# Optimization experiments

Measured on AMD Instinct MI355X. Metric: run time of the kernel, lower is better.

Reference implementation:

```python
import jax, jax.numpy as jnp
import numpy as np
from jax import lax

G, K, KS = 4, 16, 3            # stripes, latents per stripe, support kernel
TEMP, TOPK_RATIO, GATE, EPS = 0.125, 0.125, 0.05, 1e-6


def _l2norm(v):
    # F.normalize(p=2, dim=-1): divide by max(norm, 1e-12)
    return v / jnp.maximum(jnp.linalg.norm(v, axis=-1, keepdims=True), 1e-12)


def _avg_pool3(x):
    # 3x3 avg pool, stride 1, pad 1, count_include_pad=True (torch default)
    s = lax.reduce_window(x, 0.0, lax.add, (1, 1, KS, KS), (1, 1, 1, 1),
                          [(0, 0), (0, 0), (KS // 2, KS // 2), (KS // 2, KS // 2)])
    return s / float(KS * KS)


def setup_inputs() -> dict:
    key = jax.random.key(0)
    k1, k2 = jax.random.split(key)
    x = jax.random.normal(k1, (64, 256, 64, 44), dtype=jnp.float32)
    latent_basis = jax.random.normal(k2, (G, K, 256), dtype=jnp.float32) * 0.05
    return {"x": x, "latent_basis": latent_basis}


def reference(x, latent_basis):
    n, c, h, w = x.shape
    hs = h // G
    # 'n c (g hs) w -> (n g) c hs w'
    sf = x.reshape(n, c, G, hs, w).transpose(0, 2, 1, 3, 4).reshape(n * G, c, hs, w)
    support_feat = _avg_pool3(sf)
    feat_flat = sf.reshape(n, G, c, hs * w).transpose(0, 1, 3, 2)          # n g p c
    supp_flat = support_feat.reshape(n, G, c, hs * w).transpose(0, 1, 3, 2)  # n g p c
    # active mask from detached energy
    e = jnp.mean(lax.stop_gradient(sf) ** 2, axis=1)                       # [n*G, hs, w]
    e = e / jnp.maximum(jnp.max(e, axis=(-2, -1), keepdims=True), EPS)
    am = (e > GATE).astype(jnp.float32)
    fb = (e > 0).astype(jnp.float32)
    use_fb = jnp.sum(am, axis=(-2, -1), keepdims=True) <= 0
    am = jnp.where(use_fb, fb, am).reshape(n, G, hs * w)                   # n g p
    # routing
    sfn = _l2norm(supp_flat)
    lb = _l2norm(latent_basis)                                             # g k c
    logits = jnp.einsum('ngpc,gkc->ngpk', sfn, lb) / TEMP
    route = jax.nn.softmax(logits, axis=-1)
    supp = route * am[..., None]                                           # n g p k
    pw = supp / jnp.maximum(jnp.sum(supp, axis=2, keepdims=True), EPS)
    tokens = jnp.einsum('ngpk,ngpc->ngkc', pw, feat_flat)                  # n g k c
    tokens = tokens.transpose(0, 3, 1, 2).reshape(n, c, G * K)             # n c (g k)
    # presence via top-k over positions
    p = supp.shape[2]
    topk = max(1, min(p, int(p * TOPK_RATIO)))
    vals = lax.top_k(supp.transpose(0, 1, 3, 2), topk)[0]                  # n g k topk
    pres = jnp.mean(vals, axis=-1).reshape(n, G * K)
    pres = pres / jnp.maximum(jnp.sum(pres, axis=1, keepdims=True), EPS)
    return tokens, pres
```

## Files before the change

### kernel.cpp

```cpp
#include <hip/hip_runtime.h>
#include <cstdint>


#define C_ 256
#define W_ 44
#define P_ 704
#define CH_STRIDE 2816
#define NB_STRIDE 720896
#define TOPK_ 88
#define GATE_ 0.05f
#define EPS_ 1e-6f

#define DPP_WAVE_SHL1 0x130
#define DPP_WAVE_SHR1 0x138
__device__ __forceinline__ float dpp_from_left(float v) {
  return __int_as_float(__builtin_amdgcn_update_dpp(
      0, __float_as_int(v), DPP_WAVE_SHR1, 0xF, 0xF, true));
}
__device__ __forceinline__ float dpp_from_right(float v) {
  return __int_as_float(__builtin_amdgcn_update_dpp(
      0, __float_as_int(v), DPP_WAVE_SHL1, 0xF, 0xF, true));
}

__global__ __launch_bounds__(256) void k_norm_basis(const float* __restrict__ lb,
                                                    float* __restrict__ lbn) {
  int gk = blockIdx.x;
  int t = threadIdx.x;
  float v = lb[gk * 256 + t];
  float ss = v * v;
  #pragma unroll
  for (int off = 32; off >= 1; off >>= 1) ss += __shfl_xor(ss, off);
  __shared__ float red[4];
  if ((t & 63) == 0) red[t >> 6] = ss;
  __syncthreads();
  float tot = red[0] + red[1] + red[2] + red[3];
  float scale = 1.f / fmaxf(sqrtf(tot), 1e-12f);
  int g = gk >> 4, k = gk & 15;
  lbn[((g * 256 + t) << 4) + k] = v * scale;
}

__global__ __launch_bounds__(256) void k_route_dot(const float* __restrict__ x,
                                                   const float* __restrict__ lbn,
                                                   float* __restrict__ pd0,
                                                   float* __restrict__ pd1,
                                                   float* __restrict__ sqpw) {
  const int tid = threadIdx.x;
  const int wq = tid >> 6;
  const int l = tid & 63;
  const bool act = (l < 44);
  const int bid = blockIdx.x;
  const int s = bid >> 3;
  const int rem = bid & 7;
  const int q = rem >> 1, half = rem & 1;
  const int w = q * 4 + wq;
  const int n = s >> 2, g = s & 3;
  const int p = w * 44 + l;

  const int lsafe = act ? l : 0;
  const float* xb = x + (size_t)n * NB_STRIDE + (size_t)(half * 128) * CH_STRIDE
                      + (g * 16 + w) * 44 + lsafe;
  const float* xm = xb + ((w > 0)  ? -44 : 0);
  const float* xp = xb + ((w < 15) ?  44 : 0);
  const bool hm = (w > 0), hp = (w < 15);

  const float* lbb = lbn + (g << 12) + (half << 11);

  float rawdot[16];
  #pragma unroll
  for (int k = 0; k < 16; k++) rawdot[k] = 0.f;
  float sq = 0.f, pw2 = 0.f;

  for (int c = 0; c < 128; c += 4) {
    float vm[4], v0[4], vp[4];
    #pragma unroll
    for (int j = 0; j < 4; j++) {
      const size_t o = (size_t)(c + j) * CH_STRIDE;
      vm[j] = xm[o]; v0[j] = xb[o]; vp[j] = xp[o];
    }
    #pragma unroll
    for (int j = 0; j < 4; j++) {
      float a  = act ? v0[j] : 0.f;
      float am_ = (act && hm) ? vm[j] : 0.f;
      float ap_ = (act && hp) ? vp[j] : 0.f;
      float vs = am_ + a + ap_;
      float lf = dpp_from_left(vs);
      float rt = dpp_from_right(vs);
      float win = lf + vs + rt;
      pw2 = fmaf(win, win, pw2);
      sq  = fmaf(a, a, sq);
      const int co = __builtin_amdgcn_readfirstlane((c + j) << 4);
      const float4* wp4 = (const float4*)(lbb + co);
      float4 w0 = wp4[0], w1 = wp4[1], w2 = wp4[2], w3 = wp4[3];
      rawdot[0]  = fmaf(a, w0.x, rawdot[0]);  rawdot[1]  = fmaf(a, w0.y, rawdot[1]);
      rawdot[2]  = fmaf(a, w0.z, rawdot[2]);  rawdot[3]  = fmaf(a, w0.w, rawdot[3]);
      rawdot[4]  = fmaf(a, w1.x, rawdot[4]);  rawdot[5]  = fmaf(a, w1.y, rawdot[5]);
      rawdot[6]  = fmaf(a, w1.z, rawdot[6]);  rawdot[7]  = fmaf(a, w1.w, rawdot[7]);
      rawdot[8]  = fmaf(a, w2.x, rawdot[8]);  rawdot[9]  = fmaf(a, w2.y, rawdot[9]);
      rawdot[10] = fmaf(a, w2.z, rawdot[10]); rawdot[11] = fmaf(a, w2.w, rawdot[11]);
      rawdot[12] = fmaf(a, w3.x, rawdot[12]); rawdot[13] = fmaf(a, w3.y, rawdot[13]);
      rawdot[14] = fmaf(a, w3.z, rawdot[14]); rawdot[15] = fmaf(a, w3.w, rawdot[15]);
    }
  }

  if (act) {
    float* dst = (half ? pd1 : pd0) + (size_t)s * 11264 + p * 16;
    #pragma unroll
    for (int kq = 0; kq < 4; kq++)
      ((float4*)dst)[kq] = make_float4(rawdot[kq*4+0], rawdot[kq*4+1],
                                       rawdot[kq*4+2], rawdot[kq*4+3]);
    *(float2*)(sqpw + ((size_t)(s * 2 + half) * 704 + p) * 2) = make_float2(sq, pw2);
  }
}

__global__ __launch_bounds__(1024) void k_route_fin(float* __restrict__ supp_kp,
                                                    float* __restrict__ supp_pk,
                                                    const float* __restrict__ sqpw,
                                                    float* __restrict__ invden_ws) {
  __shared__ float rsl[11264];
  __shared__ float redA[16];
  __shared__ float redB[16];
  __shared__ float redM[2];
  __shared__ float red2[16 * 16];

  const int tid = threadIdx.x;
  const int w = tid >> 6;
  const int l = tid & 63;
  const bool act = (l < 44);
  const int s = blockIdx.x;
  const int p = w * 44 + l;

  float sq = 0.f, pw2 = 0.f;
  if (act) {
    const float4* a0 = (const float4*)(supp_kp + (size_t)s * 11264 + p * 16);
    const float4* a1 = (const float4*)(supp_pk + (size_t)s * 11264 + p * 16);
    #pragma unroll
    for (int kq = 0; kq < 4; kq++) {
      float4 u = a0[kq], v = a1[kq];
      rsl[(kq*4+0) * 704 + p] = u.x + v.x;
      rsl[(kq*4+1) * 704 + p] = u.y + v.y;
      rsl[(kq*4+2) * 704 + p] = u.z + v.z;
      rsl[(kq*4+3) * 704 + p] = u.w + v.w;
    }
    float2 s0 = *(const float2*)(sqpw + ((size_t)(s * 2 + 0) * 704 + p) * 2);
    float2 s1 = *(const float2*)(sqpw + ((size_t)(s * 2 + 1) * 704 + p) * 2);
    sq = s0.x + s1.x; pw2 = s0.y + s1.y;
  }
  __syncthreads();

  float pd[16];
  #pragma unroll
  for (int k = 0; k < 16; k++) pd[k] = 0.f;
  if (act) {
    #pragma unroll
    for (int dy = -1; dy <= 1; dy++) {
      int yy = w + dy;
      if (yy < 0 || yy > 15) continue;
      #pragma unroll
      for (int dx = -1; dx <= 1; dx++) {
        int xx = l + dx;
        if (xx < 0 || xx > 43) continue;
        int pp = yy * 44 + xx;
        #pragma unroll
        for (int k = 0; k < 16; k++) pd[k] += rsl[k * 704 + pp];
      }
    }
  }

  float e_raw = sq * (1.f / 256.f);
  float m = e_raw;
  #pragma unroll
  for (int off = 32; off >= 1; off >>= 1) m = fmaxf(m, __shfl_xor(m, off));
  if (l == 0) redA[w] = m;
  __syncthreads();
  if (tid == 0) {
    float mm = redA[0];
    for (int w2 = 1; w2 < 16; w2++) mm = fmaxf(mm, redA[w2]);
    redM[0] = mm;
  }
  __syncthreads();
  float M = fmaxf(redM[0], EPS_);
  float e = e_raw / M;
  float am = (e > GATE_) ? 1.f : 0.f;
  float fb = (e_raw > 0.f) ? 1.f : 0.f;
  float a = am;
  #pragma unroll
  for (int off = 32; off >= 1; off >>= 1) a += __shfl_xor(a, off);
  if (l == 0) redB[w] = a;
  __syncthreads();
  if (tid == 0) {
    float sm = 0.f;
    for (int w2 = 0; w2 < 16; w2++) sm += redB[w2];
    redM[1] = sm;
  }
  __syncthreads();
  if (redM[1] <= 0.f) am = fb;

  float pnorm = sqrtf(pw2) * (1.f / 9.f);
  float invn = 1.f / fmaxf(pnorm, 1e-12f);
  float scl = invn * (8.f / 9.f);
  float li[16];
  float mx = -1e30f;
  #pragma unroll
  for (int k = 0; k < 16; k++) { li[k] = pd[k] * scl; mx = fmaxf(mx, li[k]); }
  float ssum = 0.f;
  #pragma unroll
  for (int k = 0; k < 16; k++) { li[k] = __expf(li[k] - mx); ssum += li[k]; }
  float rs2 = am / ssum;
  float supp[16];
  #pragma unroll
  for (int k = 0; k < 16; k++) supp[k] = li[k] * rs2;

  if (act) {
    float* sbp = supp_kp + (size_t)s * (16 * 704);
    #pragma unroll
    for (int k = 0; k < 16; k++) sbp[k * 704 + p] = supp[k];
    float* spk = supp_pk + ((size_t)s * 704 + p) * 16;
    #pragma unroll
    for (int kq = 0; kq < 4; kq++)
      ((float4*)spk)[kq] = make_float4(supp[kq*4+0], supp[kq*4+1],
                                       supp[kq*4+2], supp[kq*4+3]);
  }

  #pragma unroll
  for (int k = 0; k < 16; k++) {
    float v2 = act ? supp[k] : 0.f;
    #pragma unroll
    for (int off = 32; off >= 1; off >>= 1) v2 += __shfl_xor(v2, off);
    if (l == 0) red2[w * 16 + k] = v2;
  }
  __syncthreads();
  if (tid < 16) {
    float den = 0.f;
    for (int w2 = 0; w2 < 16; w2++) den += red2[w2 * 16 + tid];
    invden_ws[s * 16 + tid] = 1.f / fmaxf(den, EPS_);
  }
}

__global__ __launch_bounds__(256) void k_topk(const float* __restrict__ supp_kp,
                                              float* __restrict__ presraw) {
  const int blk = blockIdx.x;
  const int t = threadIdx.x;
  const int lane = t & 63, w = t >> 6;
  const float* v = supp_kp + (size_t)blk * 704;
  const bool h2 = (t < 192);
  uint32_t key0 = __float_as_uint(v[t]);
  uint32_t key1 = __float_as_uint(v[t + 256]);
  uint32_t key2 = h2 ? __float_as_uint(v[t + 512]) : 0u;

  __shared__ uint32_t hist[256];
  __shared__ uint32_t sarr[257];
  __shared__ uint32_t wsum[4];
  __shared__ uint32_t bc0, bc1;
  uint32_t prefix = 0, remaining = TOPK_;

  for (int b = 3; b >= 0; b--) {
    hist[t] = 0u;
    __syncthreads();
    const int shift = b * 8;
    uint32_t mhi = (b == 3) ? 0u : (0xFFFFFFFFu << (shift + 8));
    if ((key0 & mhi) == (prefix & mhi)) atomicAdd(&hist[(key0 >> shift) & 255u], 1u);
    if ((key1 & mhi) == (prefix & mhi)) atomicAdd(&hist[(key1 >> shift) & 255u], 1u);
    if (h2 && ((key2 & mhi) == (prefix & mhi))) atomicAdd(&hist[(key2 >> shift) & 255u], 1u);
    __syncthreads();

    uint32_t val = hist[t];
    #pragma unroll
    for (int off = 1; off < 64; off <<= 1) {
      uint32_t o = (uint32_t)__shfl_down((int)val, off);
      if (lane + off < 64) val += o;
    }
    if (lane == 0) wsum[w] = val;
    __syncthreads();
    uint32_t add = 0;
    for (int w2 = w + 1; w2 < 4; w2++) add += wsum[w2];
    sarr[t] = val + add;
    if (t == 0) sarr[256] = 0u;
    __syncthreads();
    uint32_t s_t = sarr[t], s_n = sarr[t + 1];
    if (s_t >= remaining && s_n < remaining) {
      bc0 = prefix | ((uint32_t)t << shift);
      bc1 = remaining - s_n;
    }
    __syncthreads();
    prefix = bc0; remaining = bc1;
    __syncthreads();
  }

  float tf = __uint_as_float(prefix);
  float sgt = 0.f;
  uint32_t cgt = 0;
  if (key0 > prefix) { sgt += __uint_as_float(key0); cgt++; }
  if (key1 > prefix) { sgt += __uint_as_float(key1); cgt++; }
  if (h2 && key2 > prefix) { sgt += __uint_as_float(key2); cgt++; }
  #pragma unroll
  for (int off = 32; off >= 1; off >>= 1) {
    sgt += __shfl_xor(sgt, off);
    cgt += __shfl_xor(cgt, off);
  }
  __shared__ float rsx[4];
  __shared__ uint32_t rcx[4];
  if (lane == 0) { rsx[w] = sgt; rcx[w] = cgt; }
  __syncthreads();
  if (t == 0) {
    float stot = rsx[0] + rsx[1] + rsx[2] + rsx[3];
    uint32_t ctot = rcx[0] + rcx[1] + rcx[2] + rcx[3];
    float top = stot + (float)(TOPK_ - ctot) * tf;
    presraw[blk] = top * (1.f / (float)TOPK_);
  }
}

__global__ __launch_bounds__(512, 4) void k_tokens(const float* __restrict__ x,
                                                   const float* __restrict__ supp_pk,
                                                   const float* __restrict__ invden,
                                                   float* __restrict__ out) {
  __shared__ float xl[4096];
  const int tid = threadIdx.x;
  const int bid = blockIdx.x;
  const int s = bid >> 1, chalf = bid & 1;
  const int n = s >> 2, g = s & 3;
  const int cl = tid & 127;
  const int q = tid >> 7;
  const int sblk = s * (704 * 16);

  const float* xs = x + (size_t)n * NB_STRIDE + (size_t)(chalf * 128) * CH_STRIDE + g * P_;

  const int li0 = tid, li1 = tid + 512;
  const int lc0 = li0 >> 3, lj0 = li0 & 7;
  const int lc1 = li1 >> 3, lj1 = li1 & 7;
  const float* gp0 = xs + (size_t)lc0 * CH_STRIDE + lj0 * 4;
  const float* gp1 = xs + (size_t)lc1 * CH_STRIDE + lj1 * 4;
  const int wo0 = lc0 * 32 + ((lj0 * 4) ^ ((lc0 & 7) * 4));
  const int wo1 = lc1 * 32 + ((lj1 * 4) ^ ((lc1 & 7) * 4));

  const int sw = (cl & 7) * 4;
  const int rbase = cl * 32;

  float acc[16];
  #pragma unroll
  for (int k = 0; k < 16; k++) acc[k] = 0.f;

  float4 r0 = *(const float4*)gp0;
  float4 r1 = *(const float4*)gp1;
  *(float4*)&xl[wo0] = r0;
  *(float4*)&xl[wo1] = r1;
  __syncthreads();

  for (int tt = 0; tt < 22; tt++) {
    const int p0 = tt * 32;
    float4 n0, n1;
    if (tt < 21) {
      n0 = *(const float4*)(gp0 + p0 + 32);
      n1 = *(const float4*)(gp1 + p0 + 32);
    }

    #pragma unroll
    for (int jj = 0; jj < 8; jj += 4) {
      const int pp0 = q * 8 + jj;
      float4 xv = *(const float4*)&xl[rbase + (pp0 ^ sw)];
      float xa[4] = {xv.x, xv.y, xv.z, xv.w};
      #pragma unroll
      for (int dj = 0; dj < 4; dj++) {
        int uofs = __builtin_amdgcn_readfirstlane(sblk + (p0 + pp0 + dj) * 16);
        const float4* sp = (const float4*)(supp_pk + uofs);
        float4 s0 = sp[0], s1 = sp[1], s2 = sp[2], s3 = sp[3];
        float a = xa[dj];
        acc[0]  += a * s0.x; acc[1]  += a * s0.y; acc[2]  += a * s0.z; acc[3]  += a * s0.w;
        acc[4]  += a * s1.x; acc[5]  += a * s1.y; acc[6]  += a * s1.z; acc[7]  += a * s1.w;
        acc[8]  += a * s2.x; acc[9]  += a * s2.y; acc[10] += a * s2.z; acc[11] += a * s2.w;
        acc[12] += a * s3.x; acc[13] += a * s3.y; acc[14] += a * s3.z; acc[15] += a * s3.w;
      }
    }

    __syncthreads();
    if (tt < 21) {
      *(float4*)&xl[wo0] = n0;
      *(float4*)&xl[wo1] = n1;
      __syncthreads();
    }
  }

  if (q >= 2) {
    float* dst = &xl[((q - 2) * 128 + cl) * 16];
    #pragma unroll
    for (int kq = 0; kq < 4; kq++)
      ((float4*)dst)[kq] = make_float4(acc[kq*4], acc[kq*4+1], acc[kq*4+2], acc[kq*4+3]);
  }
  __syncthreads();
  if (q < 2) {
    const float* src = &xl[(q * 128 + cl) * 16];
    #pragma unroll
    for (int k = 0; k < 16; k++) acc[k] += src[k];
  }
  __syncthreads();
  if (q == 1) {
    float* dst = &xl[cl * 16];
    #pragma unroll
    for (int kq = 0; kq < 4; kq++)
      ((float4*)dst)[kq] = make_float4(acc[kq*4], acc[kq*4+1], acc[kq*4+2], acc[kq*4+3]);
  }
  __syncthreads();
  if (q == 0) {
    const float* src = &xl[cl * 16];
    float* op = out + ((size_t)(n * 256 + chalf * 128 + cl) * 64) + g * 16;
    #pragma unroll
    for (int kq = 0; kq < 4; kq++) {
      int u = __builtin_amdgcn_readfirstlane(s * 16 + kq * 4);
      const float4 iv = *(const float4*)(invden + u);
      float4 o;
      o.x = (acc[kq*4+0] + src[kq*4+0]) * iv.x;
      o.y = (acc[kq*4+1] + src[kq*4+1]) * iv.y;
      o.z = (acc[kq*4+2] + src[kq*4+2]) * iv.z;
      o.w = (acc[kq*4+3] + src[kq*4+3]) * iv.w;
      ((float4*)op)[kq] = o;
    }
  }
}

__global__ __launch_bounds__(64) void k_pres(const float* __restrict__ presraw,
                                             float* __restrict__ out) {
  const int n = blockIdx.x, t = threadIdx.x;
  float v = presraw[n * 64 + t];
  float ssum = v;
  #pragma unroll
  for (int off = 32; off >= 1; off >>= 1) ssum += __shfl_xor(ssum, off);
  out[1048576 + n * 64 + t] = v / fmaxf(ssum, EPS_);
}

extern "C" void kernel_launch(void* const* d_in, const int* in_sizes, int n_in,
                              void* d_out, int out_size, void* d_ws, size_t ws_size,
                              hipStream_t stream) {
  (void)in_sizes; (void)n_in; (void)out_size; (void)ws_size;
  const float* x  = (const float*)d_in[0];
  const float* lb = (const float*)d_in[1];
  float* out = (float*)d_out;
  float* ws = (float*)d_ws;
  float* lbn_ws     = ws;
  float* invden_ws  = ws + 16384;
  float* presraw_ws = ws + 20480;
  float* supp_kp_ws = ws + 24576;
  float* supp_pk_ws = ws + 2908160;
  float* sqpw_ws    = out;

  k_norm_basis<<<64, 256, 0, stream>>>(lb, lbn_ws);
  k_route_dot<<<2048, 256, 0, stream>>>(x, lbn_ws, supp_kp_ws, supp_pk_ws, sqpw_ws);
  k_route_fin<<<256, 1024, 0, stream>>>(supp_kp_ws, supp_pk_ws, sqpw_ws, invden_ws);
  k_topk<<<4096, 256, 0, stream>>>(supp_kp_ws, presraw_ws);
  k_tokens<<<512, 512, 0, stream>>>(x, supp_pk_ws, invden_ws, out);
  k_pres<<<64, 64, 0, stream>>>(presraw_ws, out);
}
```

Baseline: 370.6 us.

## Fuse top-k presence into route_fin and software-pipeline route_dot channel loads

Removes the separate k_topk kernel. Each wave of k_route_fin now runs an 8-bit radix select over one latent's 704 support values. It keeps the values in shared memory and uses a wave-private histogram with shuffle-based scans instead of block-wide barriers. This also drops the global write of the k-major support buffer and its later re-read. Separately, k_route_dot double-buffers its channel-group loads and adds an occupancy hint in launch_bounds to hide global memory latency. The cost is more shared memory per route_fin block and more register pressure in route_dot.

```diff
diff --git a/kernel.cpp b/kernel.cpp
--- a/kernel.cpp
+++ b/kernel.cpp
@@ -39,11 +39,43 @@
   lbn[((g * 256 + t) << 4) + k] = v * scale;
 }
 
-__global__ __launch_bounds__(256) void k_route_dot(const float* __restrict__ x,
-                                                   const float* __restrict__ lbn,
-                                                   float* __restrict__ pd0,
-                                                   float* __restrict__ pd1,
-                                                   float* __restrict__ sqpw) {
+#define LOAD_GRP(Pm, P0, Pp, cbase)                                    \
+  { _Pragma("unroll")                                                  \
+    for (int j_ = 0; j_ < 4; j_++) {                                   \
+      const size_t o_ = (size_t)((cbase) + j_) * CH_STRIDE;            \
+      Pm[j_] = xm[o_]; P0[j_] = xb[o_]; Pp[j_] = xp[o_];               \
+    } }
+
+#define CONS_GRP(Pm, P0, Pp, cbase)                                    \
+  { _Pragma("unroll")                                                  \
+    for (int j_ = 0; j_ < 4; j_++) {                                   \
+      float a  = act ? P0[j_] : 0.f;                                   \
+      float am_ = (act && hm) ? Pm[j_] : 0.f;                          \
+      float ap_ = (act && hp) ? Pp[j_] : 0.f;                          \
+      float vs = am_ + a + ap_;                                        \
+      float lf = dpp_from_left(vs);                                    \
+      float rt = dpp_from_right(vs);                                   \
+      float win = lf + vs + rt;                                        \
+      pw2 = fmaf(win, win, pw2);                                       \
+      sq  = fmaf(a, a, sq);                                            \
+      const int co_ = __builtin_amdgcn_readfirstlane(((cbase) + j_) << 4); \
+      const float4* wp4 = (const float4*)(lbb + co_);                  \
+      float4 w0 = wp4[0], w1 = wp4[1], w2 = wp4[2], w3 = wp4[3];       \
+      rawdot[0]  = fmaf(a, w0.x, rawdot[0]);  rawdot[1]  = fmaf(a, w0.y, rawdot[1]);  \
+      rawdot[2]  = fmaf(a, w0.z, rawdot[2]);  rawdot[3]  = fmaf(a, w0.w, rawdot[3]);  \
+      rawdot[4]  = fmaf(a, w1.x, rawdot[4]);  rawdot[5]  = fmaf(a, w1.y, rawdot[5]);  \
+      rawdot[6]  = fmaf(a, w1.z, rawdot[6]);  rawdot[7]  = fmaf(a, w1.w, rawdot[7]);  \
+      rawdot[8]  = fmaf(a, w2.x, rawdot[8]);  rawdot[9]  = fmaf(a, w2.y, rawdot[9]);  \
+      rawdot[10] = fmaf(a, w2.z, rawdot[10]); rawdot[11] = fmaf(a, w2.w, rawdot[11]); \
+      rawdot[12] = fmaf(a, w3.x, rawdot[12]); rawdot[13] = fmaf(a, w3.y, rawdot[13]); \
+      rawdot[14] = fmaf(a, w3.z, rawdot[14]); rawdot[15] = fmaf(a, w3.w, rawdot[15]); \
+    } }
+
+__global__ __launch_bounds__(256, 4) void k_route_dot(const float* __restrict__ x,
+                                                      const float* __restrict__ lbn,
+                                                      float* __restrict__ pd0,
+                                                      float* __restrict__ pd1,
+                                                      float* __restrict__ sqpw) {
   const int tid = threadIdx.x;
   const int wq = tid >> 6;
   const int l = tid & 63;
@@ -70,36 +102,15 @@
   for (int k = 0; k < 16; k++) rawdot[k] = 0.f;
   float sq = 0.f, pw2 = 0.f;
 
-  for (int c = 0; c < 128; c += 4) {
-    float vm[4], v0[4], vp[4];
-    #pragma unroll
-    for (int j = 0; j < 4; j++) {
-      const size_t o = (size_t)(c + j) * CH_STRIDE;
-      vm[j] = xm[o]; v0[j] = xb[o]; vp[j] = xp[o];
-    }
-    #pragma unroll
-    for (int j = 0; j < 4; j++) {
-      float a  = act ? v0[j] : 0.f;
-      float am_ = (act && hm) ? vm[j] : 0.f;
-      float ap_ = (act && hp) ? vp[j] : 0.f;
-      float vs = am_ + a + ap_;
-      float lf = dpp_from_left(vs);
-      float rt = dpp_from_right(vs);
-      float win = lf + vs + rt;
-      pw2 = fmaf(win, win, pw2);
-      sq  = fmaf(a, a, sq);
-      const int co = __builtin_amdgcn_readfirstlane((c + j) << 4);
-      const float4* wp4 = (const float4*)(lbb + co);
-      float4 w0 = wp4[0], w1 = wp4[1], w2 = wp4[2], w3 = wp4[3];
-      rawdot[0]  = fmaf(a, w0.x, rawdot[0]);  rawdot[1]  = fmaf(a, w0.y, rawdot[1]);
-      rawdot[2]  = fmaf(a, w0.z, rawdot[2]);  rawdot[3]  = fmaf(a, w0.w, rawdot[3]);
-      rawdot[4]  = fmaf(a, w1.x, rawdot[4]);  rawdot[5]  = fmaf(a, w1.y, rawdot[5]);
-      rawdot[6]  = fmaf(a, w1.z, rawdot[6]);  rawdot[7]  = fmaf(a, w1.w, rawdot[7]);
-      rawdot[8]  = fmaf(a, w2.x, rawdot[8]);  rawdot[9]  = fmaf(a, w2.y, rawdot[9]);
-      rawdot[10] = fmaf(a, w2.z, rawdot[10]); rawdot[11] = fmaf(a, w2.w, rawdot[11]);
-      rawdot[12] = fmaf(a, w3.x, rawdot[12]); rawdot[13] = fmaf(a, w3.y, rawdot[13]);
-      rawdot[14] = fmaf(a, w3.z, rawdot[14]); rawdot[15] = fmaf(a, w3.w, rawdot[15]);
-    }
+  float Avm[4], Av0[4], Avp[4];
+  float Bvm[4], Bv0[4], Bvp[4];
+
+  LOAD_GRP(Avm, Av0, Avp, 0)
+  for (int c = 0; c < 128; c += 8) {
+    LOAD_GRP(Bvm, Bv0, Bvp, c + 4)
+    CONS_GRP(Avm, Av0, Avp, c)
+    if (c + 8 < 128) { LOAD_GRP(Avm, Av0, Avp, c + 8) }
+    CONS_GRP(Bvm, Bv0, Bvp, c + 4)
   }
 
   if (act) {
@@ -112,11 +123,14 @@
   }
 }
 
-__global__ __launch_bounds__(1024) void k_route_fin(float* __restrict__ supp_kp,
+__global__ __launch_bounds__(1024) void k_route_fin(const float* __restrict__ pd0,
+                                                    const float* __restrict__ pd1,
+                                                    const float* __restrict__ sqpw,
                                                     float* __restrict__ supp_pk,
-                                                    const float* __restrict__ sqpw,
-                                                    float* __restrict__ invden_ws) {
+                                                    float* __restrict__ invden_ws,
+                                                    float* __restrict__ presraw) {
   __shared__ float rsl[11264];
+  __shared__ uint32_t hist_l[16 * 256];
   __shared__ float redA[16];
   __shared__ float redB[16];
   __shared__ float redM[2];
@@ -131,8 +145,8 @@
 
   float sq = 0.f, pw2 = 0.f;
   if (act) {
-    const float4* a0 = (const float4*)(supp_kp + (size_t)s * 11264 + p * 16);
-    const float4* a1 = (const float4*)(supp_pk + (size_t)s * 11264 + p * 16);
+    const float4* a0 = (const float4*)(pd0 + (size_t)s * 11264 + p * 16);
+    const float4* a1 = (const float4*)(pd1 + (size_t)s * 11264 + p * 16);
     #pragma unroll
     for (int kq = 0; kq < 4; kq++) {
       float4 u = a0[kq], v = a1[kq];
@@ -211,9 +225,6 @@
   for (int k = 0; k < 16; k++) supp[k] = li[k] * rs2;
 
   if (act) {
-    float* sbp = supp_kp + (size_t)s * (16 * 704);
-    #pragma unroll
-    for (int k = 0; k < 16; k++) sbp[k * 704 + p] = supp[k];
     float* spk = supp_pk + ((size_t)s * 704 + p) * 16;
     #pragma unroll
     for (int kq = 0; kq < 4; kq++)
@@ -234,78 +245,62 @@
     for (int w2 = 0; w2 < 16; w2++) den += red2[w2 * 16 + tid];
     invden_ws[s * 16 + tid] = 1.f / fmaxf(den, EPS_);
   }
-}
-
-__global__ __launch_bounds__(256) void k_topk(const float* __restrict__ supp_kp,
-                                              float* __restrict__ presraw) {
-  const int blk = blockIdx.x;
-  const int t = threadIdx.x;
-  const int lane = t & 63, w = t >> 6;
-  const float* v = supp_kp + (size_t)blk * 704;
-  const bool h2 = (t < 192);
-  uint32_t key0 = __float_as_uint(v[t]);
-  uint32_t key1 = __float_as_uint(v[t + 256]);
-  uint32_t key2 = h2 ? __float_as_uint(v[t + 512]) : 0u;
-
-  __shared__ uint32_t hist[256];
-  __shared__ uint32_t sarr[257];
-  __shared__ uint32_t wsum[4];
-  __shared__ uint32_t bc0, bc1;
-  uint32_t prefix = 0, remaining = TOPK_;
-
-  for (int b = 3; b >= 0; b--) {
-    hist[t] = 0u;
-    __syncthreads();
-    const int shift = b * 8;
-    uint32_t mhi = (b == 3) ? 0u : (0xFFFFFFFFu << (shift + 8));
-    if ((key0 & mhi) == (prefix & mhi)) atomicAdd(&hist[(key0 >> shift) & 255u], 1u);
-    if ((key1 & mhi) == (prefix & mhi)) atomicAdd(&hist[(key1 >> shift) & 255u], 1u);
-    if (h2 && ((key2 & mhi) == (prefix & mhi))) atomicAdd(&hist[(key2 >> shift) & 255u], 1u);
-    __syncthreads();
-
-    uint32_t val = hist[t];
-    #pragma unroll
-    for (int off = 1; off < 64; off <<= 1) {
-      uint32_t o = (uint32_t)__shfl_down((int)val, off);
-      if (lane + off < 64) val += o;
-    }
-    if (lane == 0) wsum[w] = val;
-    __syncthreads();
-    uint32_t add = 0;
-    for (int w2 = w + 1; w2 < 4; w2++) add += wsum[w2];
-    sarr[t] = val + add;
-    if (t == 0) sarr[256] = 0u;
-    __syncthreads();
-    uint32_t s_t = sarr[t], s_n = sarr[t + 1];
-    if (s_t >= remaining && s_n < remaining) {
-      bc0 = prefix | ((uint32_t)t << shift);
-      bc1 = remaining - s_n;
-    }
-    __syncthreads();
-    prefix = bc0; remaining = bc1;
-    __syncthreads();
-  }
-
-  float tf = __uint_as_float(prefix);
-  float sgt = 0.f;
-  uint32_t cgt = 0;
-  if (key0 > prefix) { sgt += __uint_as_float(key0); cgt++; }
-  if (key1 > prefix) { sgt += __uint_as_float(key1); cgt++; }
-  if (h2 && key2 > prefix) { sgt += __uint_as_float(key2); cgt++; }
-  #pragma unroll
-  for (int off = 32; off >= 1; off >>= 1) {
-    sgt += __shfl_xor(sgt, off);
-    cgt += __shfl_xor(cgt, off);
-  }
-  __shared__ float rsx[4];
-  __shared__ uint32_t rcx[4];
-  if (lane == 0) { rsx[w] = sgt; rcx[w] = cgt; }
-  __syncthreads();
-  if (t == 0) {
-    float stot = rsx[0] + rsx[1] + rsx[2] + rsx[3];
-    uint32_t ctot = rcx[0] + rcx[1] + rcx[2] + rcx[3];
-    float top = stot + (float)(TOPK_ - ctot) * tf;
-    presraw[blk] = top * (1.f / (float)TOPK_);
+
+  if (act) {
+    #pragma unroll
+    for (int k = 0; k < 16; k++) rsl[k * 704 + p] = supp[k];
+  }
+  __syncthreads();
+
+  {
+    const int k = w;
+    uint32_t key[11];
+    #pragma unroll
+    for (int j = 0; j < 11; j++)
+      key[j] = __float_as_uint(rsl[k * 704 + l + 64 * j]);
+    uint32_t* h = &hist_l[w * 256];
+    uint32_t prefix = 0, remaining = TOPK_;
+    #pragma unroll
+    for (int b = 3; b >= 0; b--) {
+      const int shift = b * 8;
+      *(uint4*)&h[l * 4] = make_uint4(0u, 0u, 0u, 0u);
+      uint32_t mhi = (b == 3) ? 0u : (0xFFFFFFFFu << (shift + 8));
+      #pragma unroll
+      for (int j = 0; j < 11; j++)
+        if ((key[j] & mhi) == (prefix & mhi))
+          atomicAdd(&h[(key[j] >> shift) & 255u], 1u);
+      uint4 bn = *(uint4*)&h[l * 4];
+      uint32_t T = bn.x + bn.y + bn.z + bn.w;
+      uint32_t inc = T;
+      #pragma unroll
+      for (int off = 1; off < 64; off <<= 1) {
+        uint32_t o = (uint32_t)__shfl_down((int)inc, off);
+        if (l + off < 64) inc += o;
+      }
+      uint32_t excl = inc - T;
+      uint32_t g3 = excl + bn.w, g2 = g3 + bn.z, g1 = g2 + bn.y, g0 = g1 + bn.x;
+      uint32_t pk = 0u;
+      if (g0 >= remaining && g1 < remaining) pk = ((uint32_t)(4*l+0) << 16) | (remaining - g1);
+      if (g1 >= remaining && g2 < remaining) pk = ((uint32_t)(4*l+1) << 16) | (remaining - g2);
+      if (g2 >= remaining && g3 < remaining) pk = ((uint32_t)(4*l+2) << 16) | (remaining - g3);
+      if (g3 >= remaining && excl < remaining) pk = ((uint32_t)(4*l+3) << 16) | (remaining - excl);
+      #pragma unroll
+      for (int off = 32; off >= 1; off >>= 1) pk |= (uint32_t)__shfl_xor((int)pk, off);
+      prefix |= ((pk >> 16) & 255u) << shift;
+      remaining = pk & 0xFFFFu;
+    }
+    float tf = __uint_as_float(prefix);
+    float sgt = 0.f; uint32_t cgt = 0u;
+    #pragma unroll
+    for (int j = 0; j < 11; j++)
+      if (key[j] > prefix) { sgt += __uint_as_float(key[j]); cgt++; }
+    #pragma unroll
+    for (int off = 32; off >= 1; off >>= 1) {
+      sgt += __shfl_xor(sgt, off);
+      cgt += (uint32_t)__shfl_xor((int)cgt, off);
+    }
+    if (l == 0)
+      presraw[s * 16 + k] = (sgt + (float)(TOPK_ - cgt) * tf) * (1.f / (float)TOPK_);
   }
 }
 
@@ -443,8 +438,8 @@
 
   k_norm_basis<<<64, 256, 0, stream>>>(lb, lbn_ws);
   k_route_dot<<<2048, 256, 0, stream>>>(x, lbn_ws, supp_kp_ws, supp_pk_ws, sqpw_ws);
-  k_route_fin<<<256, 1024, 0, stream>>>(supp_kp_ws, supp_pk_ws, sqpw_ws, invden_ws);
-  k_topk<<<4096, 256, 0, stream>>>(supp_kp_ws, presraw_ws);
+  k_route_fin<<<256, 1024, 0, stream>>>(supp_kp_ws, supp_pk_ws, sqpw_ws,
+                                        supp_pk_ws, invden_ws, presraw_ws);
   k_tokens<<<512, 512, 0, stream>>>(x, supp_pk_ws, invden_ws, out);
   k_pres<<<64, 64, 0, stream>>>(presraw_ws, out);
 }
```

After: 345.7 us. 1.07x faster.
